# Optimization experiments

Measured on AMD Instinct MI355X. Metric: run time of the kernel, lower is better.

The kernel has to match this reference:

```python
import jax, jax.numpy as jnp
import numpy as np

D = 512  # module_dim

def setup_inputs() -> dict:
    key = jax.random.key(0)
    ks = jax.random.split(key, 40)
    i = [0]
    def nrm(shape, scale=0.05):
        k = ks[i[0]]; i[0] += 1
        return jax.random.normal(k, shape, jnp.float32) * scale
    inp = {
        'image': nrm((32, 256, 8, 14, 14), 1.0),
        'concepts': nrm((80, D), 1.0),
        'conv1_w': nrm((D, 256, 3, 3, 3), 0.02),
        'conv1_b': jnp.zeros((D,), jnp.float32),
        'conv2_w': nrm((D, D, 3, 3, 3), 0.02),
        'conv2_b': jnp.zeros((D,), jnp.float32),
        'Wci': nrm((2 * D, D)), 'bci': jnp.zeros((D,), jnp.float32),
        'Wu': nrm((12, D, D)), 'bu': jnp.zeros((12, D), jnp.float32),
        'ctrl_attn_w': nrm((D, 1)), 'ctrl_attn_b': jnp.zeros((1,), jnp.float32),
        'Wk': nrm((D, D)), 'bk': jnp.zeros((D,), jnp.float32),
        'Wm': nrm((D, D)), 'bm': jnp.zeros((D,), jnp.float32),
        'Wcat': nrm((2 * D, D)), 'bcat': jnp.zeros((D,), jnp.float32),
        'Wcat2': nrm((D, D)), 'bcat2': jnp.zeros((D,), jnp.float32),
        'read_attn_w': nrm((D, 1)), 'read_attn_b': jnp.zeros((1,), jnp.float32),
        'Wwrite': nrm((2 * D, D)), 'bwrite': jnp.zeros((D,), jnp.float32),
        'init_control': nrm((1, D), 1.0), 'init_memory': nrm((1, D), 1.0),
        'Wproj': nrm((D, 300)), 'bproj': jnp.zeros((300,), jnp.float32),
        'out_attn_w': nrm((300, 1)), 'out_attn_b': jnp.zeros((1,), jnp.float32),
        'labels_matrix': nrm((1000, 300), 1.0),
    }
    return inp


def _conv3d(x, w, b):
    y = jax.lax.conv_general_dilated(
        x, w, window_strides=(1, 1, 1), padding='SAME',
        dimension_numbers=('NCDHW', 'OIDHW', 'NCDHW'))
    return y + b[None, :, None, None, None]


def reference(image, concepts, conv1_w, conv1_b, conv2_w, conv2_b,
              Wci, bci, Wu, bu, ctrl_attn_w, ctrl_attn_b,
              Wk, bk, Wm, bm, Wcat, bcat, Wcat2, bcat2,
              read_attn_w, read_attn_b, Wwrite, bwrite,
              init_control, init_memory, Wproj, bproj,
              out_attn_w, out_attn_b, labels_matrix):
    B = image.shape[0]
    # --- InputUnit stem (dropout is identity at eval) ---
    x = jax.nn.elu(_conv3d(image, conv1_w, conv1_b))
    x = jax.nn.elu(_conv3d(x, conv2_w, conv2_b))
    know = x.reshape(B, D, -1).transpose(0, 2, 1)      # [B, K, D]
    context = jnp.broadcast_to(concepts[None], (B,) + concepts.shape)  # [B, L, D]

    # know projection is step-invariant at eval; hoist out of the loop
    know_proj = know @ Wk + bk                          # [B, K, D]

    c0 = jnp.broadcast_to(init_control, (B, D))
    m0 = jnp.broadcast_to(init_memory, (B, D))

    def step(carry, wu):
        c, m = carry
        Wu_i, bu_i = wu
        # --- ControlUnit ---
        q = jnp.tanh(jnp.concatenate([c, m], axis=-1) @ Wci + bci)
        q = q @ Wu_i + bu_i                              # [B, D]
        cl = jnp.squeeze((q[:, None, :] * context) @ ctrl_attn_w, -1) + ctrl_attn_b
        cattn = jax.nn.softmax(cl, axis=1)               # [B, L]
        c = jnp.einsum('bl,bld->bd', cattn, context)
        # --- ReadUnit ---
        mp = m @ Wm + bm                                 # [B, D]
        inter = jnp.concatenate([know_proj * mp[:, None, :], know_proj], axis=-1)
        inter = jax.nn.elu(inter @ Wcat + bcat) @ Wcat2 + bcat2
        inter = jax.nn.elu(inter * c[:, None, :])        # [B, K, D]
        rl = jnp.squeeze(inter @ read_attn_w, -1) + read_attn_b
        rattn = jax.nn.softmax(rl, axis=1)               # [B, K]
        info = jnp.einsum('bk,bkd->bd', rattn, know)
        # --- WriteUnit ---
        m = jnp.concatenate([m, info], axis=-1) @ Wwrite + bwrite
        return (c, m), None

    (c, m), _ = jax.lax.scan(step, (c0, m0), (Wu, bu))

    # --- OutputUnit ---
    mp = m @ Wproj + bproj                               # [B, 300]
    logits = jnp.squeeze((mp[:, None, :] * labels_matrix[None]) @ out_attn_w, -1) + out_attn_b
    return jax.nn.softmax(logits, axis=1)                # [B, num_answers]
```

## Files before the change

kernel.cpp:

```cpp
#include <hip/hip_runtime.h>
#include <math.h>

#define DM    512
#define SP    1568
#define BATCH 32
#define NSTEP 12
#define CPAD  2560
#define LDT   40
#define ILS   520
#define NCH   32

typedef short s16x8 __attribute__((ext_vector_type(8)));
typedef float f32x4 __attribute__((ext_vector_type(4)));

__device__ __forceinline__ float eluf(float x) { return x > 0.f ? x : expf(x) - 1.f; }
__device__ __forceinline__ float b2f(ushort u) {
  union { float f; unsigned i; } v; v.i = ((unsigned)u) << 16; return v.f;
}
__device__ __forceinline__ ushort f2b(float f) {
  union { float f; unsigned i; } v; v.f = f;
  unsigned r = (v.i + 0x7FFFu + ((v.i >> 16) & 1u)) >> 16;
  return (ushort)r;
}

__device__ __forceinline__ void glds16(ushort* l, const ushort* g) {
  __builtin_amdgcn_global_load_lds(
      (const __attribute__((address_space(1))) void*)g,
      (__attribute__((address_space(3))) void*)l, 16, 0, 0);
}

__global__ void k_zero(uint4* __restrict__ p, long n16) {
  long stride = (long)gridDim.x * blockDim.x;
  for (long i = (long)blockIdx.x * blockDim.x + threadIdx.x; i < n16; i += stride)
    p[i] = make_uint4(0, 0, 0, 0);
}

__global__ __launch_bounds__(256) void k_padimg(const float* __restrict__ img,
                                               ushort* __restrict__ xp) {
  const int b = blockIdx.x, s0 = blockIdx.y * 32;
  __shared__ float T[256][33];
  const int t = threadIdx.x;
  const int so = t & 31, cg = t >> 5;
#pragma unroll 4
  for (int i = 0; i < 32; i++) {
    int ci = cg * 32 + i;
    T[ci][so] = img[((size_t)(b * 256 + ci)) * SP + s0 + so];
  }
  __syncthreads();
#pragma unroll 4
  for (int si = 0; si < 32; si++) {
    int s = s0 + si;
    int z = s / 196, r = s - z * 196, y = r / 14, x = r - y * 14;
    int p = (z + 1) * 256 + (y + 1) * 16 + (x + 1);
    xp[((size_t)b * CPAD + p) * 256 + t] = f2b(T[t][si]);
  }
}

template <int CIN>
__global__ __launch_bounds__(256) void k_cvtw(const float* __restrict__ w,
                                              ushort* __restrict__ o) {
  const int co = blockIdx.x;
  const int KK = 27 * CIN;
  __shared__ ushort tmp[27 * CIN];
  const int t = threadIdx.x;
  for (int i = t; i < KK; i += 256)
    tmp[i] = f2b(w[(size_t)co * KK + i]);
  __syncthreads();
  for (int i = t; i < KK; i += 256) {
    int tap = i / CIN, ci = i - tap * CIN;
    o[(size_t)co * KK + i] = tmp[ci * 27 + tap];
  }
}

__global__ void k_cvtT(const float* __restrict__ w, ushort* __restrict__ o) {
  int idx = blockIdx.x * 256 + threadIdx.x;
  int n = idx >> 9, k = idx & 511;
  o[idx] = f2b(w[(size_t)k * 512 + n]);
}

template <int CIN, int ISCONV1>
__global__ __launch_bounds__(256) void k_convm(
    const ushort* __restrict__ W, const ushort* __restrict__ Xp,
    const float* __restrict__ bias, ushort* __restrict__ Y)
{
  const int KK = CIN * 27;
  const int id = blockIdx.x;
  const int g = id & 7, r = id >> 3;
  const int b  = g * 4 + (r / 52);
  const int rr = r % 52;
  const int m0 = (rr / 13) * 128;
  const int n0 = (rr % 13) * 128;
  __shared__ __align__(16) ushort As[128 * 64];
  __shared__ __align__(16) ushort Bs[128 * 64];
  const int t = threadIdx.x;
  const int lane = t & 63, wid = t >> 6;
  const int wm = (wid >> 1) * 64, wn = (wid & 1) * 64;
  const int l15 = lane & 15, quad = lane >> 4;
  const int wrow = lane >> 3, wslot = lane & 7;

  int padrow[4]; int arow[4], gco[4];
#pragma unroll
  for (int i = 0; i < 4; i++) {
    int row = wid * 32 + i * 8 + wrow;
    arow[i] = row;
    gco[i] = (wslot ^ (row & 7)) * 8;
    int n = n0 + row;
    if (n >= SP) n = SP - 1;
    int z = n / 196, rm = n - z * 196, y = rm / 14, x = rm - y * 14;
    padrow[i] = z * 256 + y * 16 + x;
  }

  f32x4 acc[4][4];
#pragma unroll
  for (int i = 0; i < 4; i++)
#pragma unroll
    for (int j = 0; j < 4; j++) acc[i][j] = (f32x4){0.f, 0.f, 0.f, 0.f};

  for (int k0 = 0; k0 < KK; k0 += 64) {
#pragma unroll
    for (int i = 0; i < 4; i++)
      glds16(&As[(wid * 32 + i * 8) * 64],
             &W[(size_t)(m0 + arow[i]) * KK + k0 + gco[i]]);
    {
      int tap = k0 / CIN, ci0 = k0 - tap * CIN;
      int dz = tap / 9, rr2 = tap - dz * 9, dy = rr2 / 3, dx = rr2 - dy * 3;
      int tofs = dz * 256 + dy * 16 + dx;
      const ushort* src = Xp + (size_t)b * CPAD * CIN + ci0;
#pragma unroll
      for (int i = 0; i < 4; i++)
        glds16(&Bs[(wid * 32 + i * 8) * 64],
               &src[(size_t)(padrow[i] + tofs) * CIN + gco[i]]);
    }
    __syncthreads();
#pragma unroll
    for (int sub = 0; sub < 2; sub++) {
      s16x8 af[4], bfr[4];
#pragma unroll
      for (int i = 0; i < 4; i++) {
        int row = wm + i * 16 + l15;
        int c = sub * 4 + quad;
        af[i] = *(const s16x8*)&As[row * 64 + ((c ^ (row & 7)) * 8)];
      }
#pragma unroll
      for (int j = 0; j < 4; j++) {
        int row = wn + j * 16 + l15;
        int c = sub * 4 + quad;
        bfr[j] = *(const s16x8*)&Bs[row * 64 + ((c ^ (row & 7)) * 8)];
      }
#pragma unroll
      for (int i = 0; i < 4; i++)
#pragma unroll
        for (int j = 0; j < 4; j++)
          acc[i][j] = __builtin_amdgcn_mfma_f32_16x16x32_bf16(af[i], bfr[j], acc[i][j], 0, 0, 0);
    }
    __syncthreads();
  }

  int nout[4]; size_t obase[4];
#pragma unroll
  for (int j = 0; j < 4; j++) {
    int n = n0 + wn + j * 16 + l15;
    nout[j] = n; obase[j] = 0;
    if (n < SP) {
      if (ISCONV1) {
        int z = n / 196, rm = n - z * 196, y = rm / 14, x = rm - y * 14;
        obase[j] = ((size_t)b * CPAD + z * 256 + y * 16 + x + 273) * 512;
      } else {
        obase[j] = ((size_t)b * SP + n) * DM;
      }
    }
  }
#pragma unroll
  for (int i = 0; i < 4; i++) {
    int cob = m0 + wm + i * 16 + quad * 4;
    float4 bb = *(const float4*)&bias[cob];
#pragma unroll
    for (int j = 0; j < 4; j++) {
      if (nout[j] < SP) {
        ushort4 o;
        o.x = f2b(eluf(acc[i][j][0] + bb.x));
        o.y = f2b(eluf(acc[i][j][1] + bb.y));
        o.z = f2b(eluf(acc[i][j][2] + bb.z));
        o.w = f2b(eluf(acc[i][j][3] + bb.w));
        *(ushort4*)&Y[obase[j] + cob] = o;
      }
    }
  }
}

__global__ __launch_bounds__(256) void k_gemmm(
    const ushort* __restrict__ A0, const ushort* __restrict__ Bt,
    const float* __restrict__ bias, ushort* __restrict__ Cv)
{
  const int id = blockIdx.x;
  const int g = id & 7, r = id >> 3;
  const int bq = g * 4 + (r / 52);
  const int rr = r % 52;
  const int n0 = (rr / 13) * 128;
  const int m0 = (rr % 13) * 128;
  const ushort* A = A0 + (size_t)bq * SP * DM;
  __shared__ __align__(16) ushort As[128 * LDT];
  __shared__ __align__(16) ushort Bs[128 * LDT];
  const int t = threadIdx.x;
  const int lane = t & 63, wid = t >> 6;
  const int wm = (wid >> 1) * 64, wn = (wid & 1) * 64;
  const int l15 = lane & 15, quad = lane >> 4;
  f32x4 acc[4][4];
#pragma unroll
  for (int i = 0; i < 4; i++)
#pragma unroll
    for (int j = 0; j < 4; j++) acc[i][j] = (f32x4){0.f, 0.f, 0.f, 0.f};

  for (int k0 = 0; k0 < DM; k0 += 32) {
#pragma unroll
    for (int i = 0; i < 2; i++) {
      int f = t + i * 256;
      int row = f >> 2, ko = (f & 3) * 8;
      int mg = m0 + row;
      uint4 v = make_uint4(0, 0, 0, 0);
      if (mg < SP) v = *(const uint4*)&A[(size_t)mg * DM + k0 + ko];
      *(uint4*)&As[row * LDT + ko] = v;
      uint4 w = *(const uint4*)&Bt[(size_t)(n0 + row) * DM + k0 + ko];
      *(uint4*)&Bs[row * LDT + ko] = w;
    }
    __syncthreads();
    s16x8 af[4], bfr[4];
#pragma unroll
    for (int i = 0; i < 4; i++)
      af[i] = *(const s16x8*)&As[(wm + i * 16 + l15) * LDT + quad * 8];
#pragma unroll
    for (int j = 0; j < 4; j++)
      bfr[j] = *(const s16x8*)&Bs[(wn + j * 16 + l15) * LDT + quad * 8];
#pragma unroll
    for (int i = 0; i < 4; i++)
#pragma unroll
      for (int j = 0; j < 4; j++)
        acc[i][j] = __builtin_amdgcn_mfma_f32_16x16x32_bf16(af[i], bfr[j], acc[i][j], 0, 0, 0);
    __syncthreads();
  }

  ushort* C = Cv + (size_t)bq * SP * DM;
#pragma unroll
  for (int j = 0; j < 4; j++) {
    int n = n0 + wn + j * 16 + l15;
    float bb = bias[n];
#pragma unroll
    for (int i = 0; i < 4; i++) {
      int mb = m0 + wm + i * 16 + quad * 4;
#pragma unroll
      for (int r2 = 0; r2 < 4; r2++) {
        int m = mb + r2;
        if (m < SP) C[(size_t)m * DM + n] = f2b(acc[i][j][r2] + bb);
      }
    }
  }
}

__global__ __launch_bounds__(1024, 4) void k_fused12(
    const ushort* __restrict__ kproj, const ushort* __restrict__ befft,
    const ushort* __restrict__ wc2t, const float* __restrict__ bcat,
    const float* __restrict__ bcat2, const float* __restrict__ cbuf,
    const float* __restrict__ raw, float* __restrict__ rl)
{
  extern __shared__ __align__(16) char smem[];
  ushort* Af  = (ushort*)smem;
  ushort* Il  = Af + 64 * ILS;
  float*  red = (float*)(Il + 64 * ILS);

  const int tile = blockIdx.x;
  const int g = tile & 7, r = tile >> 3;
  const int b  = g * 4 + (r / 25);
  const int m0 = (r % 25) * 64;
  const int t  = threadIdx.x;
  const int lane = t & 63, w = t >> 6;
  const int l15 = lane & 15, quad = lane >> 4;

  const ushort* kpb = kproj + (size_t)b * SP * DM;
#pragma unroll
  for (int i = 0; i < 4; i++) {
    int f = t + i * 1024;
    int row = f >> 6, ch = (f & 63) * 8;
    int mg = m0 + row;
    uint4 v = make_uint4(0, 0, 0, 0);
    if (mg < SP) v = *(const uint4*)&kpb[(size_t)mg * DM + ch];
    *(uint4*)&Af[row * ILS + ch] = v;
  }
  __syncthreads();

  const ushort* bfb = befft + (size_t)b * DM * DM;
  {
    f32x4 acc[4][2];
#pragma unroll
    for (int i = 0; i < 4; i++)
#pragma unroll
      for (int j = 0; j < 2; j++) acc[i][j] = (f32x4){0.f, 0.f, 0.f, 0.f};
#pragma unroll 2
    for (int k0 = 0; k0 < DM; k0 += 32) {
      s16x8 bf[2], af[4];
#pragma unroll
      for (int j = 0; j < 2; j++)
        bf[j] = *(const s16x8*)&bfb[(size_t)(w * 32 + j * 16 + l15) * DM + k0 + quad * 8];
#pragma unroll
      for (int i = 0; i < 4; i++)
        af[i] = *(const s16x8*)&Af[(i * 16 + l15) * ILS + k0 + quad * 8];
#pragma unroll
      for (int i = 0; i < 4; i++)
#pragma unroll
        for (int j = 0; j < 2; j++)
          acc[i][j] = __builtin_amdgcn_mfma_f32_16x16x32_bf16(af[i], bf[j], acc[i][j], 0, 0, 0);
    }
#pragma unroll
    for (int j = 0; j < 2; j++) {
      int n1 = w * 32 + j * 16 + l15;
      float bc = bcat[n1];
#pragma unroll
      for (int i = 0; i < 4; i++)
#pragma unroll
        for (int r2 = 0; r2 < 4; r2++)
          Il[(i * 16 + quad * 4 + r2) * ILS + n1] = f2b(eluf(acc[i][j][r2] + bc));
    }
  }
  __syncthreads();

  f32x4 acc2[4][2];
#pragma unroll
  for (int i = 0; i < 4; i++)
#pragma unroll
    for (int j = 0; j < 2; j++) acc2[i][j] = (f32x4){0.f, 0.f, 0.f, 0.f};
#pragma unroll 2
  for (int kk = 0; kk < DM; kk += 32) {
    s16x8 af[4], bf[2];
#pragma unroll
    for (int i = 0; i < 4; i++)
      af[i] = *(const s16x8*)&Il[(i * 16 + l15) * ILS + kk + quad * 8];
#pragma unroll
    for (int j = 0; j < 2; j++)
      bf[j] = *(const s16x8*)&wc2t[(size_t)(w * 32 + j * 16 + l15) * DM + kk + quad * 8];
#pragma unroll
    for (int i = 0; i < 4; i++)
#pragma unroll
      for (int j = 0; j < 2; j++)
        acc2[i][j] = __builtin_amdgcn_mfma_f32_16x16x32_bf16(af[i], bf[j], acc2[i][j], 0, 0, 0);
  }

  float epi[16];
#pragma unroll
  for (int e = 0; e < 16; e++) epi[e] = 0.f;
#pragma unroll
  for (int j = 0; j < 2; j++) {
    int n2 = w * 32 + j * 16 + l15;
    float b2 = bcat2[n2], cc = cbuf[(size_t)b * DM + n2], rw = raw[n2];
#pragma unroll
    for (int i = 0; i < 4; i++)
#pragma unroll
      for (int r2 = 0; r2 < 4; r2++)
        epi[i * 4 + r2] += eluf((acc2[i][j][r2] + b2) * cc) * rw;
  }
#pragma unroll
  for (int d2 = 1; d2 < 16; d2 <<= 1)
#pragma unroll
    for (int e = 0; e < 16; e++) epi[e] += __shfl_xor(epi[e], d2, 64);
  if (l15 == 0) {
#pragma unroll
    for (int i = 0; i < 4; i++)
#pragma unroll
      for (int r2 = 0; r2 < 4; r2++)
        red[(i * 16 + quad * 4 + r2) * 16 + w] = epi[i * 4 + r2];
  }
  __syncthreads();
  if (t < 64) {
    int m = m0 + t;
    if (m < SP) {
      float s = 0.f;
#pragma unroll
      for (int q = 0; q < 16; q++) s += red[t * 16 + q];
      rl[(size_t)b * SP + m] = s;
    }
  }
}

__global__ __launch_bounds__(256) void k_prefold(
    const float* __restrict__ Wcat, const float* __restrict__ mp,
    ushort* __restrict__ Bf)
{
  const int k0 = blockIdx.x * 64, n0 = blockIdx.y * 64;
  const int bbase = blockIdx.z * 8;
  __shared__ float S1[64][68], S2[64][68];
  const int t = threadIdx.x;
#pragma unroll
  for (int i = 0; i < 4; i++) {
    int f = t + i * 256;
    int kk = f >> 4, nn2 = (f & 15) * 4;
    float4 a = *(const float4*)&Wcat[(size_t)(k0 + kk) * DM + n0 + nn2];
    float4 c = *(const float4*)&Wcat[(size_t)(DM + k0 + kk) * DM + n0 + nn2];
    *(float4*)&S1[kk][nn2] = a;
    *(float4*)&S2[kk][nn2] = c;
  }
  __syncthreads();
  const int n = t >> 2, kseg = (t & 3) * 16;
  for (int bq = 0; bq < 8; bq++) {
    const float* mpb = mp + (size_t)(bbase + bq) * DM + k0 + kseg;
    ushort* out = Bf + ((size_t)(bbase + bq) * DM + n0 + n) * DM + k0 + kseg;
#pragma unroll
    for (int g = 0; g < 4; g++) {
      ushort4 o;
      o.x = f2b(mpb[g * 4 + 0] * S1[kseg + g * 4 + 0][n] + S2[kseg + g * 4 + 0][n]);
      o.y = f2b(mpb[g * 4 + 1] * S1[kseg + g * 4 + 1][n] + S2[kseg + g * 4 + 1][n]);
      o.z = f2b(mpb[g * 4 + 2] * S1[kseg + g * 4 + 2][n] + S2[kseg + g * 4 + 2][n]);
      o.w = f2b(mpb[g * 4 + 3] * S1[kseg + g * 4 + 3][n] + S2[kseg + g * 4 + 3][n]);
      *(ushort4*)&out[g * 4] = o;
    }
  }
}

__global__ __launch_bounds__(512) void k_ctrl(
    const float* cin, const float* __restrict__ min_,
    const float* __restrict__ Wci, const float* __restrict__ bci,
    const float* __restrict__ Wu_i, const float* __restrict__ bu_i,
    const float* __restrict__ caw, const float* __restrict__ concepts,
    const float* __restrict__ Wm, const float* __restrict__ bm,
    float* cout, float* __restrict__ mpout)
{
  const int b = blockIdx.x, t = threadIdx.x;
  __shared__ float sc[512], sm[512], sq0[512], sqa[512], scl[80], red[512];
  sc[t] = cin[b * DM + t];
  sm[t] = min_[b * DM + t];
  __syncthreads();
  {
    const int d = t;
    float a0 = bci[d], a1 = 0.f, a2 = 0.f, a3 = 0.f;
    for (int k = 0; k < 512; k += 4) {
      a0 = fmaf(sc[k + 0], Wci[(size_t)(k + 0) * DM + d], a0);
      a1 = fmaf(sc[k + 1], Wci[(size_t)(k + 1) * DM + d], a1);
      a2 = fmaf(sc[k + 2], Wci[(size_t)(k + 2) * DM + d], a2);
      a3 = fmaf(sc[k + 3], Wci[(size_t)(k + 3) * DM + d], a3);
    }
    for (int k = 0; k < 512; k += 4) {
      a0 = fmaf(sm[k + 0], Wci[(size_t)(512 + k + 0) * DM + d], a0);
      a1 = fmaf(sm[k + 1], Wci[(size_t)(512 + k + 1) * DM + d], a1);
      a2 = fmaf(sm[k + 2], Wci[(size_t)(512 + k + 2) * DM + d], a2);
      a3 = fmaf(sm[k + 3], Wci[(size_t)(512 + k + 3) * DM + d], a3);
    }
    sq0[d] = tanhf((a0 + a1) + (a2 + a3));
    float p0 = bm[d], p1 = 0.f, p2 = 0.f, p3 = 0.f;
    for (int k = 0; k < 512; k += 4) {
      p0 = fmaf(sm[k + 0], Wm[(size_t)(k + 0) * DM + d], p0);
      p1 = fmaf(sm[k + 1], Wm[(size_t)(k + 1) * DM + d], p1);
      p2 = fmaf(sm[k + 2], Wm[(size_t)(k + 2) * DM + d], p2);
      p3 = fmaf(sm[k + 3], Wm[(size_t)(k + 3) * DM + d], p3);
    }
    mpout[b * DM + d] = (p0 + p1) + (p2 + p3);
  }
  __syncthreads();
  {
    const int d = t;
    float a0 = bu_i[d], a1 = 0.f, a2 = 0.f, a3 = 0.f;
    for (int k = 0; k < 512; k += 4) {
      a0 = fmaf(sq0[k + 0], Wu_i[(size_t)(k + 0) * DM + d], a0);
      a1 = fmaf(sq0[k + 1], Wu_i[(size_t)(k + 1) * DM + d], a1);
      a2 = fmaf(sq0[k + 2], Wu_i[(size_t)(k + 2) * DM + d], a2);
      a3 = fmaf(sq0[k + 3], Wu_i[(size_t)(k + 3) * DM + d], a3);
    }
    sqa[d] = ((a0 + a1) + (a2 + a3)) * caw[d];
  }
  __syncthreads();
  float myl = -INFINITY;
  if (t < 80) {
    float a0 = 0.f, a1 = 0.f, a2 = 0.f, a3 = 0.f;
    for (int d = 0; d < 512; d += 4) {
      a0 = fmaf(sqa[d + 0], concepts[(size_t)t * DM + d + 0], a0);
      a1 = fmaf(sqa[d + 1], concepts[(size_t)t * DM + d + 1], a1);
      a2 = fmaf(sqa[d + 2], concepts[(size_t)t * DM + d + 2], a2);
      a3 = fmaf(sqa[d + 3], concepts[(size_t)t * DM + d + 3], a3);
    }
    float a = (a0 + a1) + (a2 + a3);
    scl[t] = a; myl = a;
  }
  red[t] = myl; __syncthreads();
  for (int s = 256; s > 0; s >>= 1) { if (t < s) red[t] = fmaxf(red[t], red[t + s]); __syncthreads(); }
  float mx = red[0]; __syncthreads();
  float e = 0.f;
  if (t < 80) e = expf(scl[t] - mx);
  red[t] = e; __syncthreads();
  for (int s = 256; s > 0; s >>= 1) { if (t < s) red[t] += red[t + s]; __syncthreads(); }
  float inv = 1.f / red[0]; __syncthreads();
  if (t < 80) scl[t] = e * inv;
  __syncthreads();
  {
    const int d = t;
    float a0 = 0.f, a1 = 0.f, a2 = 0.f, a3 = 0.f;
    for (int l = 0; l < 80; l += 4) {
      a0 = fmaf(scl[l + 0], concepts[(size_t)(l + 0) * DM + d], a0);
      a1 = fmaf(scl[l + 1], concepts[(size_t)(l + 1) * DM + d], a1);
      a2 = fmaf(scl[l + 2], concepts[(size_t)(l + 2) * DM + d], a2);
      a3 = fmaf(scl[l + 3], concepts[(size_t)(l + 3) * DM + d], a3);
    }
    cout[b * DM + d] = (a0 + a1) + (a2 + a3);
  }
}

__global__ __launch_bounds__(256) void k_softinfo(
    const float* __restrict__ rl, const ushort* __restrict__ know,
    float* __restrict__ ipart)
{
  const int b = blockIdx.x, c = blockIdx.y, t = threadIdx.x;
  __shared__ float red[256];
  __shared__ float rprob[49];
  float vals[7]; float vmax = -INFINITY;
#pragma unroll
  for (int q = 0; q < 7; q++) {
    int s = t + q * 256;
    float v = (s < SP) ? rl[(size_t)b * SP + s] : -INFINITY;
    vals[q] = v; vmax = fmaxf(vmax, v);
  }
  red[t] = vmax; __syncthreads();
  for (int s = 128; s > 0; s >>= 1) { if (t < s) red[t] = fmaxf(red[t], red[t + s]); __syncthreads(); }
  float mx = red[0]; __syncthreads();
  float lsum = 0.f;
#pragma unroll
  for (int q = 0; q < 7; q++) {
    int s = t + q * 256;
    lsum += (s < SP) ? expf(vals[q] - mx) : 0.f;
  }
  red[t] = lsum; __syncthreads();
  for (int s = 128; s > 0; s >>= 1) { if (t < s) red[t] += red[t + s]; __syncthreads(); }
  float inv = 1.f / red[0];

  if (t < 49) rprob[t] = expf(rl[(size_t)b * SP + c * 49 + t] - mx) * inv;
  __syncthreads();

  float a0 = 0.f, a1 = 0.f;
  const ushort* kb = know + (size_t)b * SP * DM + (size_t)c * 49 * DM + 2 * t;
  for (int si = 0; si < 49; si++) {
    float r = rprob[si];
    ushort2 kv = *(const ushort2*)&kb[(size_t)si * DM];
    a0 = fmaf(r, b2f(kv.x), a0);
    a1 = fmaf(r, b2f(kv.y), a1);
  }
  ipart[((size_t)b * NCH + c) * DM + 2 * t] = a0;
  ipart[((size_t)b * NCH + c) * DM + 2 * t + 1] = a1;
}

__global__ __launch_bounds__(256) void k_write(
    const float* __restrict__ mold, const float* __restrict__ ipart,
    const float* __restrict__ Ww, const float* __restrict__ bw,
    float* __restrict__ mnew)
{
  const int b = blockIdx.x, half = blockIdx.y, t = threadIdx.x;
  __shared__ float smo[512], sinfo[512];
  for (int k = t; k < 512; k += 256) {
    smo[k] = mold[b * DM + k];
    float s0 = 0.f, s1 = 0.f, s2 = 0.f, s3 = 0.f;
    for (int c = 0; c < NCH; c += 4) {
      s0 += ipart[((size_t)b * NCH + c + 0) * DM + k];
      s1 += ipart[((size_t)b * NCH + c + 1) * DM + k];
      s2 += ipart[((size_t)b * NCH + c + 2) * DM + k];
      s3 += ipart[((size_t)b * NCH + c + 3) * DM + k];
    }
    sinfo[k] = (s0 + s1) + (s2 + s3);
  }
  __syncthreads();
  int d = half * 256 + t;
  float a0 = bw[d], a1 = 0.f, a2 = 0.f, a3 = 0.f;
  for (int k = 0; k < 512; k += 4) {
    a0 = fmaf(smo[k + 0], Ww[(size_t)(k + 0) * DM + d], a0);
    a1 = fmaf(smo[k + 1], Ww[(size_t)(k + 1) * DM + d], a1);
    a2 = fmaf(smo[k + 2], Ww[(size_t)(k + 2) * DM + d], a2);
    a3 = fmaf(smo[k + 3], Ww[(size_t)(k + 3) * DM + d], a3);
  }
  for (int k = 0; k < 512; k += 4) {
    a0 = fmaf(sinfo[k + 0], Ww[(size_t)(512 + k + 0) * DM + d], a0);
    a1 = fmaf(sinfo[k + 1], Ww[(size_t)(512 + k + 1) * DM + d], a1);
    a2 = fmaf(sinfo[k + 2], Ww[(size_t)(512 + k + 2) * DM + d], a2);
    a3 = fmaf(sinfo[k + 3], Ww[(size_t)(512 + k + 3) * DM + d], a3);
  }
  mnew[b * DM + d] = (a0 + a1) + (a2 + a3);
}

__global__ void k_init(const float* __restrict__ initc, const float* __restrict__ initm,
                       float* __restrict__ cbuf, float* __restrict__ mbuf)
{
  const int b = blockIdx.x, t = threadIdx.x;
  cbuf[b * DM + t] = initc[t];
  mbuf[b * DM + t] = initm[t];
}

__global__ void k_mpo(const float* __restrict__ m, const float* __restrict__ Wproj,
                      const float* __restrict__ bproj, const float* __restrict__ ow,
                      float* __restrict__ mw)
{
  const int b = blockIdx.x, t = threadIdx.x;
  __shared__ float smem[512];
  for (int k = t; k < 512; k += 320) smem[k] = m[b * DM + k];
  __syncthreads();
  if (t < 300) {
    float a0 = bproj[t], a1 = 0.f, a2 = 0.f, a3 = 0.f;
    for (int k = 0; k < 512; k += 4) {
      a0 = fmaf(smem[k + 0], Wproj[(size_t)(k + 0) * 300 + t], a0);
      a1 = fmaf(smem[k + 1], Wproj[(size_t)(k + 1) * 300 + t], a1);
      a2 = fmaf(smem[k + 2], Wproj[(size_t)(k + 2) * 300 + t], a2);
      a3 = fmaf(smem[k + 3], Wproj[(size_t)(k + 3) * 300 + t], a3);
    }
    mw[b * 300 + t] = ((a0 + a1) + (a2 + a3)) * ow[t];
  }
}

__global__ void k_logits(const float* __restrict__ mw, const float* __restrict__ labels,
                         float* __restrict__ logits)
{
  const int b = blockIdx.x, t = threadIdx.x;
  const int a = blockIdx.y * 256 + t;
  __shared__ float smw[300];
  for (int p = t; p < 300; p += 256) smw[p] = mw[b * 300 + p];
  __syncthreads();
  if (a < 1000) {
    float a0 = 0.f, a1 = 0.f, a2 = 0.f, a3 = 0.f;
    for (int p = 0; p < 300; p += 4) {
      a0 = fmaf(smw[p + 0], labels[(size_t)a * 300 + p + 0], a0);
      a1 = fmaf(smw[p + 1], labels[(size_t)a * 300 + p + 1], a1);
      a2 = fmaf(smw[p + 2], labels[(size_t)a * 300 + p + 2], a2);
      a3 = fmaf(smw[p + 3], labels[(size_t)a * 300 + p + 3], a3);
    }
    logits[b * 1000 + a] = (a0 + a1) + (a2 + a3);
  }
}

__global__ void k_softmax_out(const float* __restrict__ logits, float* __restrict__ out)
{
  const int b = blockIdx.x, t = threadIdx.x;
  __shared__ float red[256];
  float v[4]; float vmax = -INFINITY;
#pragma unroll
  for (int q = 0; q < 4; q++) {
    int a = t + q * 256;
    v[q] = (a < 1000) ? logits[b * 1000 + a] : -INFINITY;
    vmax = fmaxf(vmax, v[q]);
  }
  red[t] = vmax; __syncthreads();
  for (int s = 128; s > 0; s >>= 1) { if (t < s) red[t] = fmaxf(red[t], red[t + s]); __syncthreads(); }
  float mx = red[0]; __syncthreads();
  float lsum = 0.f;
#pragma unroll
  for (int q = 0; q < 4; q++) {
    int a = t + q * 256;
    v[q] = (a < 1000) ? expf(v[q] - mx) : 0.f;
    lsum += v[q];
  }
  red[t] = lsum; __syncthreads();
  for (int s = 128; s > 0; s >>= 1) { if (t < s) red[t] += red[t + s]; __syncthreads(); }
  float inv = 1.f / red[0];
#pragma unroll
  for (int q = 0; q < 4; q++) {
    int a = t + q * 256;
    if (a < 1000) out[b * 1000 + a] = v[q] * inv;
  }
}

extern "C" void kernel_launch(void* const* d_in, const int* in_sizes, int n_in,
                              void* d_out, int out_size, void* d_ws, size_t ws_size,
                              hipStream_t stream)
{
  const float* image    = (const float*)d_in[0];
  const float* concepts = (const float*)d_in[1];
  const float* conv1_w  = (const float*)d_in[2];
  const float* conv1_b  = (const float*)d_in[3];
  const float* conv2_w  = (const float*)d_in[4];
  const float* conv2_b  = (const float*)d_in[5];
  const float* Wci      = (const float*)d_in[6];
  const float* bci      = (const float*)d_in[7];
  const float* Wu       = (const float*)d_in[8];
  const float* bu       = (const float*)d_in[9];
  const float* caw      = (const float*)d_in[10];
  const float* Wk       = (const float*)d_in[12];
  const float* bk       = (const float*)d_in[13];
  const float* Wm       = (const float*)d_in[14];
  const float* bm       = (const float*)d_in[15];
  const float* Wcat     = (const float*)d_in[16];
  const float* bcat     = (const float*)d_in[17];
  const float* Wcat2    = (const float*)d_in[18];
  const float* bcat2    = (const float*)d_in[19];
  const float* raw      = (const float*)d_in[20];
  const float* Wwrite   = (const float*)d_in[22];
  const float* bwrite   = (const float*)d_in[23];
  const float* initc    = (const float*)d_in[24];
  const float* initm    = (const float*)d_in[25];
  const float* Wproj    = (const float*)d_in[26];
  const float* bproj    = (const float*)d_in[27];
  const float* oaw      = (const float*)d_in[28];
  const float* labels   = (const float*)d_in[30];

  char* ws = (char*)d_ws;
  const size_t OFF_KNOW = 0;
  const size_t OFF_XPAD = 51380224;
  const size_t SZ_XPAD  = 83951616;
  const size_t OFF_W    = OFF_XPAD + SZ_XPAD;
  const size_t OFF_WKT  = OFF_W + 14155776;
  const size_t OFF_WC2T = OFF_WKT + 524288;
  size_t off = OFF_WC2T + 524288;
  auto allocB = [&](size_t bytes) {
    void* p = ws + off; off += (bytes + 255) & ~(size_t)255; return p;
  };
  ushort* know   = (ushort*)(ws + OFF_KNOW);
  ushort* imgpad = (ushort*)(ws + OFF_KNOW);
  ushort* xpad1  = (ushort*)(ws + OFF_XPAD);
  ushort* kproj  = (ushort*)(ws + OFF_XPAD);
  ushort* befft  = (ushort*)(ws + OFF_XPAD + 51380224);
  float*  rl     = (float*) (ws + OFF_XPAD + 68157440);
  ushort* w1b    = (ushort*)(ws + OFF_W);
  ushort* w2b    = (ushort*)(ws + OFF_W);
  ushort* wkt    = (ushort*)(ws + OFF_WKT);
  ushort* wc2t   = (ushort*)(ws + OFF_WC2T);
  float* ipart  = (float*)allocB((size_t)BATCH * NCH * DM * 4);
  float* cbuf   = (float*)allocB(BATCH * DM * 4);
  float* mbufA  = (float*)allocB(BATCH * DM * 4);
  float* mbufB  = (float*)allocB(BATCH * DM * 4);
  float* mp     = (float*)allocB(BATCH * DM * 4);
  float* mw     = (float*)allocB(BATCH * 300 * 4);
  float* logits = (float*)allocB(BATCH * 1000 * 4);
  if (off > ws_size) return;

  const int FUSED_LDS = 64 * ILS * 2 * 2 + 64 * 16 * 4;
  hipFuncSetAttribute((const void*)k_fused12,
                      hipFuncAttributeMaxDynamicSharedMemorySize, FUSED_LDS);

  k_zero<<<4096, 256, 0, stream>>>((uint4*)imgpad, 2625536L);
  k_zero<<<4096, 256, 0, stream>>>((uint4*)xpad1, 5246976L);
  k_padimg<<<dim3(BATCH, 49), 256, 0, stream>>>(image, imgpad);
  k_cvtw<256><<<512, 256, 0, stream>>>(conv1_w, w1b);
  k_cvtT<<<1024, 256, 0, stream>>>(Wk, wkt);
  k_cvtT<<<1024, 256, 0, stream>>>(Wcat2, wc2t);
  k_convm<256, 1><<<1664, 256, 0, stream>>>(w1b, imgpad, conv1_b, xpad1);
  k_cvtw<512><<<512, 256, 0, stream>>>(conv2_w, w2b);
  k_convm<512, 0><<<1664, 256, 0, stream>>>(w2b, xpad1, conv2_b, know);
  k_gemmm<<<1664, 256, 0, stream>>>(know, wkt, bk, kproj);
  k_init<<<BATCH, DM, 0, stream>>>(initc, initm, cbuf, mbufA);

  float* mc = mbufA; float* mn = mbufB;
  for (int i = 0; i < NSTEP; i++) {
    k_ctrl<<<BATCH, 512, 0, stream>>>(cbuf, mc, Wci, bci,
                                      Wu + (size_t)i * DM * DM, bu + i * DM,
                                      caw, concepts, Wm, bm, cbuf, mp);
    k_prefold<<<dim3(8, 8, 4), 256, 0, stream>>>(Wcat, mp, befft);
    k_fused12<<<dim3(800), 1024, FUSED_LDS, stream>>>(
        kproj, befft, wc2t, bcat, bcat2, cbuf, raw, rl);
    k_softinfo<<<dim3(BATCH, NCH), 256, 0, stream>>>(rl, know, ipart);
    k_write<<<dim3(BATCH, 2), 256, 0, stream>>>(mc, ipart, Wwrite, bwrite, mn);
    float* tswap = mc; mc = mn; mn = tswap;
  }

  k_mpo<<<BATCH, 320, 0, stream>>>(mc, Wproj, bproj, oaw, mw);
  k_logits<<<dim3(BATCH, 4), 256, 0, stream>>>(mw, labels, logits);
  k_softmax_out<<<BATCH, 256, 0, stream>>>(logits, (float*)d_out);

  (void)in_sizes; (void)n_in; (void)out_size;
}
```

Measured before the change: 5.005 ms.

## Restructure control and write matvecs as batched GEMMs sharing weight loads

The per-batch control and write kernels, where each block re-read the full weight matrices, are split into kernels in which each thread computes four output columns for one batch element. Weights are read once with float4 loads and shared across all 32 batch rows, using transposed [D,32] state buffers kept alongside the row-major copies. The aim is to stop re-reading the weights 32 times, since the small recurrent matvecs are bound by weight traffic. The cost is more kernel launches per step, extra transposed state buffers, only 16 blocks for the GEMM kernels, and non-coalesced scattered stores of the transposed outputs.

```diff
diff --git a/kernel.cpp b/kernel.cpp
--- a/kernel.cpp
+++ b/kernel.cpp
@@ -413,56 +413,72 @@
   }
 }
 
-__global__ __launch_bounds__(512) void k_ctrl(
-    const float* cin, const float* __restrict__ min_,
+__global__ __launch_bounds__(256) void k_ctrlA(
+    const float* __restrict__ cT, const float* __restrict__ mT,
     const float* __restrict__ Wci, const float* __restrict__ bci,
-    const float* __restrict__ Wu_i, const float* __restrict__ bu_i,
-    const float* __restrict__ caw, const float* __restrict__ concepts,
     const float* __restrict__ Wm, const float* __restrict__ bm,
-    float* cout, float* __restrict__ mpout)
+    float* __restrict__ q0T, float* __restrict__ mp)
+{
+  const int t = threadIdx.x;
+  const int b = t & 31, g = t >> 5;
+  const int d0 = blockIdx.x * 32 + g * 4;
+  float4 acc = make_float4(0.f, 0.f, 0.f, 0.f);
+  float4 pac = make_float4(0.f, 0.f, 0.f, 0.f);
+  for (int k = 0; k < 512; k++) {
+    float a = cT[k * 32 + b];
+    float4 w = *(const float4*)&Wci[(size_t)k * DM + d0];
+    acc.x = fmaf(a, w.x, acc.x); acc.y = fmaf(a, w.y, acc.y);
+    acc.z = fmaf(a, w.z, acc.z); acc.w = fmaf(a, w.w, acc.w);
+  }
+  for (int k = 0; k < 512; k++) {
+    float a = mT[k * 32 + b];
+    float4 w = *(const float4*)&Wci[(size_t)(512 + k) * DM + d0];
+    acc.x = fmaf(a, w.x, acc.x); acc.y = fmaf(a, w.y, acc.y);
+    acc.z = fmaf(a, w.z, acc.z); acc.w = fmaf(a, w.w, acc.w);
+    float4 wm = *(const float4*)&Wm[(size_t)k * DM + d0];
+    pac.x = fmaf(a, wm.x, pac.x); pac.y = fmaf(a, wm.y, pac.y);
+    pac.z = fmaf(a, wm.z, pac.z); pac.w = fmaf(a, wm.w, pac.w);
+  }
+  float4 bc = *(const float4*)&bci[d0];
+  q0T[(d0 + 0) * 32 + b] = tanhf(acc.x + bc.x);
+  q0T[(d0 + 1) * 32 + b] = tanhf(acc.y + bc.y);
+  q0T[(d0 + 2) * 32 + b] = tanhf(acc.z + bc.z);
+  q0T[(d0 + 3) * 32 + b] = tanhf(acc.w + bc.w);
+  float4 bmv = *(const float4*)&bm[d0];
+  float4 o = make_float4(pac.x + bmv.x, pac.y + bmv.y, pac.z + bmv.z, pac.w + bmv.w);
+  *(float4*)&mp[(size_t)b * DM + d0] = o;
+}
+
+__global__ __launch_bounds__(256) void k_ctrlB(
+    const float* __restrict__ q0T, const float* __restrict__ Wu_i,
+    const float* __restrict__ bu_i, const float* __restrict__ caw,
+    float* __restrict__ qa)
+{
+  const int t = threadIdx.x;
+  const int b = t & 31, g = t >> 5;
+  const int d0 = blockIdx.x * 32 + g * 4;
+  float4 acc = make_float4(0.f, 0.f, 0.f, 0.f);
+  for (int k = 0; k < 512; k++) {
+    float a = q0T[k * 32 + b];
+    float4 w = *(const float4*)&Wu_i[(size_t)k * DM + d0];
+    acc.x = fmaf(a, w.x, acc.x); acc.y = fmaf(a, w.y, acc.y);
+    acc.z = fmaf(a, w.z, acc.z); acc.w = fmaf(a, w.w, acc.w);
+  }
+  float4 bu = *(const float4*)&bu_i[d0];
+  float4 cw = *(const float4*)&caw[d0];
+  float4 o = make_float4((acc.x + bu.x) * cw.x, (acc.y + bu.y) * cw.y,
+                         (acc.z + bu.z) * cw.z, (acc.w + bu.w) * cw.w);
+  *(float4*)&qa[(size_t)b * DM + d0] = o;
+}
+
+__global__ __launch_bounds__(256) void k_ctrlC(
+    const float* __restrict__ qa, const float* __restrict__ concepts,
+    float* __restrict__ cbuf, float* __restrict__ cT)
 {
   const int b = blockIdx.x, t = threadIdx.x;
-  __shared__ float sc[512], sm[512], sq0[512], sqa[512], scl[80], red[512];
-  sc[t] = cin[b * DM + t];
-  sm[t] = min_[b * DM + t];
-  __syncthreads();
-  {
-    const int d = t;
-    float a0 = bci[d], a1 = 0.f, a2 = 0.f, a3 = 0.f;
-    for (int k = 0; k < 512; k += 4) {
-      a0 = fmaf(sc[k + 0], Wci[(size_t)(k + 0) * DM + d], a0);
-      a1 = fmaf(sc[k + 1], Wci[(size_t)(k + 1) * DM + d], a1);
-      a2 = fmaf(sc[k + 2], Wci[(size_t)(k + 2) * DM + d], a2);
-      a3 = fmaf(sc[k + 3], Wci[(size_t)(k + 3) * DM + d], a3);
-    }
-    for (int k = 0; k < 512; k += 4) {
-      a0 = fmaf(sm[k + 0], Wci[(size_t)(512 + k + 0) * DM + d], a0);
-      a1 = fmaf(sm[k + 1], Wci[(size_t)(512 + k + 1) * DM + d], a1);
-      a2 = fmaf(sm[k + 2], Wci[(size_t)(512 + k + 2) * DM + d], a2);
-      a3 = fmaf(sm[k + 3], Wci[(size_t)(512 + k + 3) * DM + d], a3);
-    }
-    sq0[d] = tanhf((a0 + a1) + (a2 + a3));
-    float p0 = bm[d], p1 = 0.f, p2 = 0.f, p3 = 0.f;
-    for (int k = 0; k < 512; k += 4) {
-      p0 = fmaf(sm[k + 0], Wm[(size_t)(k + 0) * DM + d], p0);
-      p1 = fmaf(sm[k + 1], Wm[(size_t)(k + 1) * DM + d], p1);
-      p2 = fmaf(sm[k + 2], Wm[(size_t)(k + 2) * DM + d], p2);
-      p3 = fmaf(sm[k + 3], Wm[(size_t)(k + 3) * DM + d], p3);
-    }
-    mpout[b * DM + d] = (p0 + p1) + (p2 + p3);
-  }
-  __syncthreads();
-  {
-    const int d = t;
-    float a0 = bu_i[d], a1 = 0.f, a2 = 0.f, a3 = 0.f;
-    for (int k = 0; k < 512; k += 4) {
-      a0 = fmaf(sq0[k + 0], Wu_i[(size_t)(k + 0) * DM + d], a0);
-      a1 = fmaf(sq0[k + 1], Wu_i[(size_t)(k + 1) * DM + d], a1);
-      a2 = fmaf(sq0[k + 2], Wu_i[(size_t)(k + 2) * DM + d], a2);
-      a3 = fmaf(sq0[k + 3], Wu_i[(size_t)(k + 3) * DM + d], a3);
-    }
-    sqa[d] = ((a0 + a1) + (a2 + a3)) * caw[d];
-  }
+  __shared__ float sqa[512], scl[80], red[256];
+  sqa[t] = qa[(size_t)b * DM + t];
+  sqa[t + 256] = qa[(size_t)b * DM + t + 256];
   __syncthreads();
   float myl = -INFINITY;
   if (t < 80) {
@@ -477,17 +493,18 @@
     scl[t] = a; myl = a;
   }
   red[t] = myl; __syncthreads();
-  for (int s = 256; s > 0; s >>= 1) { if (t < s) red[t] = fmaxf(red[t], red[t + s]); __syncthreads(); }
+  for (int s = 128; s > 0; s >>= 1) { if (t < s) red[t] = fmaxf(red[t], red[t + s]); __syncthreads(); }
   float mx = red[0]; __syncthreads();
   float e = 0.f;
   if (t < 80) e = expf(scl[t] - mx);
   red[t] = e; __syncthreads();
-  for (int s = 256; s > 0; s >>= 1) { if (t < s) red[t] += red[t + s]; __syncthreads(); }
+  for (int s = 128; s > 0; s >>= 1) { if (t < s) red[t] += red[t + s]; __syncthreads(); }
   float inv = 1.f / red[0]; __syncthreads();
   if (t < 80) scl[t] = e * inv;
   __syncthreads();
-  {
-    const int d = t;
+#pragma unroll
+  for (int h = 0; h < 2; h++) {
+    int d = t + h * 256;
     float a0 = 0.f, a1 = 0.f, a2 = 0.f, a3 = 0.f;
     for (int l = 0; l < 80; l += 4) {
       a0 = fmaf(scl[l + 0], concepts[(size_t)(l + 0) * DM + d], a0);
@@ -495,7 +512,9 @@
       a2 = fmaf(scl[l + 2], concepts[(size_t)(l + 2) * DM + d], a2);
       a3 = fmaf(scl[l + 3], concepts[(size_t)(l + 3) * DM + d], a3);
     }
-    cout[b * DM + d] = (a0 + a1) + (a2 + a3);
+    float a = (a0 + a1) + (a2 + a3);
+    cbuf[(size_t)b * DM + d] = a;
+    cT[(size_t)d * 32 + b] = a;
   }
 }
 
@@ -541,48 +560,61 @@
   ipart[((size_t)b * NCH + c) * DM + 2 * t + 1] = a1;
 }
 
-__global__ __launch_bounds__(256) void k_write(
-    const float* __restrict__ mold, const float* __restrict__ ipart,
+__global__ __launch_bounds__(256) void k_red(
+    const float* __restrict__ ipart, float* __restrict__ infoT)
+{
+  const int b = blockIdx.x, t = threadIdx.x;
+  const int k = blockIdx.y * 256 + t;
+  float s0 = 0.f, s1 = 0.f, s2 = 0.f, s3 = 0.f;
+  for (int c = 0; c < NCH; c += 4) {
+    s0 += ipart[((size_t)b * NCH + c + 0) * DM + k];
+    s1 += ipart[((size_t)b * NCH + c + 1) * DM + k];
+    s2 += ipart[((size_t)b * NCH + c + 2) * DM + k];
+    s3 += ipart[((size_t)b * NCH + c + 3) * DM + k];
+  }
+  infoT[(size_t)k * 32 + b] = (s0 + s1) + (s2 + s3);
+}
+
+__global__ __launch_bounds__(256) void k_writeB(
+    const float* __restrict__ mTold, const float* __restrict__ infoT,
     const float* __restrict__ Ww, const float* __restrict__ bw,
-    float* __restrict__ mnew)
-{
-  const int b = blockIdx.x, half = blockIdx.y, t = threadIdx.x;
-  __shared__ float smo[512], sinfo[512];
-  for (int k = t; k < 512; k += 256) {
-    smo[k] = mold[b * DM + k];
-    float s0 = 0.f, s1 = 0.f, s2 = 0.f, s3 = 0.f;
-    for (int c = 0; c < NCH; c += 4) {
-      s0 += ipart[((size_t)b * NCH + c + 0) * DM + k];
-      s1 += ipart[((size_t)b * NCH + c + 1) * DM + k];
-      s2 += ipart[((size_t)b * NCH + c + 2) * DM + k];
-      s3 += ipart[((size_t)b * NCH + c + 3) * DM + k];
-    }
-    sinfo[k] = (s0 + s1) + (s2 + s3);
-  }
-  __syncthreads();
-  int d = half * 256 + t;
-  float a0 = bw[d], a1 = 0.f, a2 = 0.f, a3 = 0.f;
-  for (int k = 0; k < 512; k += 4) {
-    a0 = fmaf(smo[k + 0], Ww[(size_t)(k + 0) * DM + d], a0);
-    a1 = fmaf(smo[k + 1], Ww[(size_t)(k + 1) * DM + d], a1);
-    a2 = fmaf(smo[k + 2], Ww[(size_t)(k + 2) * DM + d], a2);
-    a3 = fmaf(smo[k + 3], Ww[(size_t)(k + 3) * DM + d], a3);
-  }
-  for (int k = 0; k < 512; k += 4) {
-    a0 = fmaf(sinfo[k + 0], Ww[(size_t)(512 + k + 0) * DM + d], a0);
-    a1 = fmaf(sinfo[k + 1], Ww[(size_t)(512 + k + 1) * DM + d], a1);
-    a2 = fmaf(sinfo[k + 2], Ww[(size_t)(512 + k + 2) * DM + d], a2);
-    a3 = fmaf(sinfo[k + 3], Ww[(size_t)(512 + k + 3) * DM + d], a3);
-  }
-  mnew[b * DM + d] = (a0 + a1) + (a2 + a3);
+    float* __restrict__ mnew, float* __restrict__ mTnew)
+{
+  const int t = threadIdx.x;
+  const int b = t & 31, g = t >> 5;
+  const int d0 = blockIdx.x * 32 + g * 4;
+  float4 acc = make_float4(0.f, 0.f, 0.f, 0.f);
+  for (int k = 0; k < 512; k++) {
+    float a = mTold[k * 32 + b];
+    float4 w = *(const float4*)&Ww[(size_t)k * DM + d0];
+    acc.x = fmaf(a, w.x, acc.x); acc.y = fmaf(a, w.y, acc.y);
+    acc.z = fmaf(a, w.z, acc.z); acc.w = fmaf(a, w.w, acc.w);
+  }
+  for (int k = 0; k < 512; k++) {
+    float a = infoT[k * 32 + b];
+    float4 w = *(const float4*)&Ww[(size_t)(512 + k) * DM + d0];
+    acc.x = fmaf(a, w.x, acc.x); acc.y = fmaf(a, w.y, acc.y);
+    acc.z = fmaf(a, w.z, acc.z); acc.w = fmaf(a, w.w, acc.w);
+  }
+  float4 bwv = *(const float4*)&bw[d0];
+  float4 o = make_float4(acc.x + bwv.x, acc.y + bwv.y, acc.z + bwv.z, acc.w + bwv.w);
+  *(float4*)&mnew[(size_t)b * DM + d0] = o;
+  mTnew[(size_t)(d0 + 0) * 32 + b] = o.x;
+  mTnew[(size_t)(d0 + 1) * 32 + b] = o.y;
+  mTnew[(size_t)(d0 + 2) * 32 + b] = o.z;
+  mTnew[(size_t)(d0 + 3) * 32 + b] = o.w;
 }
 
 __global__ void k_init(const float* __restrict__ initc, const float* __restrict__ initm,
-                       float* __restrict__ cbuf, float* __restrict__ mbuf)
+                       float* __restrict__ cbuf, float* __restrict__ mbuf,
+                       float* __restrict__ cT, float* __restrict__ mT)
 {
   const int b = blockIdx.x, t = threadIdx.x;
-  cbuf[b * DM + t] = initc[t];
-  mbuf[b * DM + t] = initm[t];
+  float c = initc[t], m = initm[t];
+  cbuf[b * DM + t] = c;
+  mbuf[b * DM + t] = m;
+  cT[(size_t)t * 32 + b] = c;
+  mT[(size_t)t * 32 + b] = m;
 }
 
 __global__ void k_mpo(const float* __restrict__ m, const float* __restrict__ Wproj,
@@ -717,6 +749,12 @@
   float* mp     = (float*)allocB(BATCH * DM * 4);
   float* mw     = (float*)allocB(BATCH * 300 * 4);
   float* logits = (float*)allocB(BATCH * 1000 * 4);
+  float* cT     = (float*)allocB(DM * 32 * 4);
+  float* mTA    = (float*)allocB(DM * 32 * 4);
+  float* mTB    = (float*)allocB(DM * 32 * 4);
+  float* q0T    = (float*)allocB(DM * 32 * 4);
+  float* qa     = (float*)allocB(BATCH * DM * 4);
+  float* infoT  = (float*)allocB(DM * 32 * 4);
   if (off > ws_size) return;
 
   const int FUSED_LDS = 64 * ILS * 2 * 2 + 64 * 16 * 4;
@@ -733,19 +771,23 @@
   k_cvtw<512><<<512, 256, 0, stream>>>(conv2_w, w2b);
   k_convm<512, 0><<<1664, 256, 0, stream>>>(w2b, xpad1, conv2_b, know);
   k_gemmm<<<1664, 256, 0, stream>>>(know, wkt, bk, kproj);
-  k_init<<<BATCH, DM, 0, stream>>>(initc, initm, cbuf, mbufA);
+  k_init<<<BATCH, DM, 0, stream>>>(initc, initm, cbuf, mbufA, cT, mTA);
 
   float* mc = mbufA; float* mn = mbufB;
+  float* mTc = mTA; float* mTn = mTB;
   for (int i = 0; i < NSTEP; i++) {
-    k_ctrl<<<BATCH, 512, 0, stream>>>(cbuf, mc, Wci, bci,
-                                      Wu + (size_t)i * DM * DM, bu + i * DM,
-                                      caw, concepts, Wm, bm, cbuf, mp);
+    k_ctrlA<<<16, 256, 0, stream>>>(cT, mTc, Wci, bci, Wm, bm, q0T, mp);
+    k_ctrlB<<<16, 256, 0, stream>>>(q0T, Wu + (size_t)i * DM * DM, bu + i * DM,
+                                    caw, qa);
+    k_ctrlC<<<BATCH, 256, 0, stream>>>(qa, concepts, cbuf, cT);
     k_prefold<<<dim3(8, 8, 4), 256, 0, stream>>>(Wcat, mp, befft);
     k_fused12<<<dim3(800), 1024, FUSED_LDS, stream>>>(
         kproj, befft, wc2t, bcat, bcat2, cbuf, raw, rl);
     k_softinfo<<<dim3(BATCH, NCH), 256, 0, stream>>>(rl, know, ipart);
-    k_write<<<dim3(BATCH, 2), 256, 0, stream>>>(mc, ipart, Wwrite, bwrite, mn);
-    float* tswap = mc; mc = mn; mn = tswap;
+    k_red<<<dim3(BATCH, 2), 256, 0, stream>>>(ipart, infoT);
+    k_writeB<<<16, 256, 0, stream>>>(mTc, infoT, Wwrite, bwrite, mn, mTn);
+    float* ts1 = mc; mc = mn; mn = ts1;
+    float* ts2 = mTc; mTc = mTn; mTn = ts2;
   }
 
   k_mpo<<<BATCH, 320, 0, stream>>>(mc, Wproj, bproj, oaw, mw);
```

Result: slower. 6.028 ms (+20.4%).
